# Kernel tuning notes

Measured on AMD Instinct MI355X. Metric: run time of the kernel, lower is better.

The kernel has to match this reference:

```python
import jax, jax.numpy as jnp
import numpy as np

B, N, H, D, L = 4, 1024, 8, 256, 4
SVD, NSP = 16, 512
DK = D // H
EPS = 1e-6


def setup_inputs() -> dict:
    key = jax.random.key(0)
    ks = jax.random.split(key, 40)
    p = {}
    p["x"] = jax.random.normal(ks[0], (B, N, D), jnp.float32)
    p["in_degrees"] = jax.random.randint(ks[1], (N,), 0, N)
    p["out_degrees"] = jax.random.randint(ks[2], (N,), 0, N)
    p["spatial_pos"] = jax.random.randint(ks[3], (N, N), 0, NSP)
    p["svd_emb"] = jax.random.normal(ks[4], (N, 2 * SVD), jnp.float32)
    # embedding tables (padding_idx=0 -> zero row)
    p["in_deg_emb"] = (0.02 * jax.random.normal(ks[5], (N, D), jnp.float32)).at[0].set(0.0)
    p["out_deg_emb"] = (0.02 * jax.random.normal(ks[6], (N, D), jnp.float32)).at[0].set(0.0)
    p["spatial_emb"] = (0.02 * jax.random.normal(ks[7], (NSP, H), jnp.float32)).at[0].set(0.0)
    # SVD linear (stored [in, out]; y = x @ W + b)
    p["W_svd"] = 0.02 * jax.random.normal(ks[8], (2 * SVD, D), jnp.float32)
    p["b_svd"] = jnp.zeros((D,), jnp.float32)
    # per-layer stacked transformer params
    names = ["Wq", "Wk", "Wv", "Wa", "W1", "W2"]
    for i, nm in enumerate(names):
        p[nm] = 0.05 * jax.random.normal(ks[9 + i], (L, D, D), jnp.float32)
    for nm in ["bq", "bk", "bv", "ba", "b1", "b2", "ln1_b", "ln2_b"]:
        p[nm] = jnp.zeros((L, D), jnp.float32)
    p["ln1_g"] = jnp.ones((L, D), jnp.float32)
    p["ln2_g"] = jnp.ones((L, D), jnp.float32)
    return p


def _ln(x, g, b):
    mu = jnp.mean(x, axis=-1, keepdims=True)
    var = jnp.mean(jnp.square(x - mu), axis=-1, keepdims=True)
    return (x - mu) * jax.lax.rsqrt(var + EPS) * g + b


def _forward(x, svd_emb, W_svd, b_svd, in_deg_emb, out_deg_emb, spatial_emb,
             Wq, bq, Wk, bk, Wv, bv, Wa, ba, ln1_g, ln1_b,
             W1, b1, W2, b2, ln2_g, ln2_b,
             in_degrees, out_degrees, spatial_pos):
    # node-level: degree embeddings ([N,D] broadcasts over batch)
    x = x + in_deg_emb[in_degrees] + out_deg_emb[out_degrees]
    # node-level: SVD embedding (deterministic sign = +1 -> concat(u, -v))
    pos = jnp.concatenate([svd_emb[:, :SVD], -svd_emb[:, SVD:]], axis=-1)
    x = x + pos @ W_svd + b_svd
    # attention-level spatial bias: [N,N,H] -> [H,N,N], broadcast over batch
    attn_bias = jnp.transpose(spatial_emb[spatial_pos], (2, 0, 1))
    scale = 1.0 / jnp.sqrt(jnp.asarray(DK, x.dtype))

    def body(h, params):
        wq, bq_, wk, bk_, wv, bv_, wa, ba_, g1, b1_, w1, bb1, w2, bb2, g2, b2_ = params
        q = (h @ wq + bq_).reshape(B, N, H, DK)
        k = (h @ wk + bk_).reshape(B, N, H, DK)
        v = (h @ wv + bv_).reshape(B, N, H, DK)
        # scores [B,H,N,N] + spatial bias [H,N,N]
        scores = jnp.einsum('bqhd,bkhd->bhqk', q, k) * scale + attn_bias
        attn = jax.nn.softmax(scores, axis=-1)
        o = jnp.einsum('bhqk,bkhd->bqhd', attn, v).reshape(B, N, D)
        h = _ln(h + o @ wa + ba_, g1, b1_)
        f = jnp.maximum(h @ w1 + bb1, 0.0) @ w2 + bb2
        h = _ln(h + f, g2, b2_)
        return h, None

    x, _ = jax.lax.scan(body, x, (Wq, bq, Wk, bk, Wv, bv, Wa, ba, ln1_g, ln1_b,
                                  W1, b1, W2, b2, ln2_g, ln2_b))
    return x


def reference(x, svd_emb, W_svd, b_svd, in_deg_emb, out_deg_emb, spatial_emb,
              Wq, bq, Wk, bk, Wv, bv, Wa, ba, ln1_g, ln1_b,
              W1, b1, W2, b2, ln2_g, ln2_b,
              in_degrees, out_degrees, spatial_pos):
    return _forward(x, svd_emb, W_svd, b_svd, in_deg_emb, out_deg_emb, spatial_emb,
                    Wq, bq, Wk, bk, Wv, bv, Wa, ba, ln1_g, ln1_b,
                    W1, b1, W2, b2, ln2_g, ln2_b,
                    in_degrees, out_degrees, spatial_pos)
```

## Files before the change

### kernel.cpp

```cpp
#include <hip/hip_runtime.h>
#include <hip/hip_bf16.h>
#include <math.h>

#define NN 1024
#define BB 4
#define HH 8
#define DD 256
#define LL 4
#define DKK 32
#define MM 4096
#define EPSF 1e-6f
#define LOG2EF 1.4426950408889634f
#define SCLOG2E 0.2550348625f

typedef __attribute__((ext_vector_type(8))) short short8;
typedef __attribute__((ext_vector_type(4))) float f32x4;
typedef unsigned int u32;

__device__ __forceinline__ unsigned short f2bf(float f) {
    __hip_bfloat16 h = __float2bfloat16(f);
    return *(unsigned short*)&h;
}
__device__ __forceinline__ float bf2f(unsigned short u) {
    unsigned v = ((unsigned)u) << 16;
    return __builtin_bit_cast(float, v);
}

__global__ __launch_bounds__(256) void init_kernel(
    const float* __restrict__ x, const int* __restrict__ deg_in,
    const int* __restrict__ deg_out, const float* __restrict__ svd,
    const float* __restrict__ in_emb, const float* __restrict__ out_emb,
    const float* __restrict__ Wsvd, const float* __restrict__ bsvd,
    const float* __restrict__ Wq, const float* __restrict__ Wk,
    const float* __restrict__ Wv, const float* __restrict__ Wa,
    const float* __restrict__ W1, const float* __restrict__ W2,
    const int* __restrict__ sp, const float* __restrict__ spemb,
    float* __restrict__ h, short* __restrict__ hb,
    short* __restrict__ Wt, short* __restrict__ bsw)
{
    int blk = blockIdx.x;
    int tid = threadIdx.x;
    {
        int n = blk & (NN - 1);
        int di = deg_in[n], dou = deg_out[n];
        float acc = x[(size_t)blk * DD + tid] + in_emb[(size_t)di * DD + tid]
                  + out_emb[(size_t)dou * DD + tid] + bsvd[tid];
        const float* sv = &svd[n * 32];
#pragma unroll
        for (int j = 0; j < 32; ++j) {
            float v = sv[j];
            v = (j < 16) ? v : -v;
            acc += v * Wsvd[j * DD + tid];
        }
        h[(size_t)blk * DD + tid] = acc;
        hb[(size_t)blk * DD + tid] = (short)f2bf(acc);
    }
    if (blk < 384) {
        __shared__ float t[64][65];
        int z = blk >> 4, tile = blk & 15;
        int name = z >> 2;
        const float* srcs[6] = {Wq, Wk, Wv, Wa, W1, W2};
        const float* W = srcs[name] + (size_t)(z & 3) * DD * DD;
        short* dst = Wt + (size_t)z * DD * DD;
        int r0 = (tile >> 2) * 64, c0 = (tile & 3) * 64;
#pragma unroll
        for (int i = 0; i < 16; ++i) {
            int idx = i * 256 + tid;
            int r = idx >> 6, cc = idx & 63;
            t[r][cc] = W[(size_t)(r0 + r) * DD + c0 + cc];
        }
        __syncthreads();
#pragma unroll
        for (int i = 0; i < 16; ++i) {
            int idx = i * 256 + tid;
            int n = idx >> 6, kk = idx & 63;
            dst[(size_t)(c0 + n) * DD + r0 + kk] = (short)f2bf(t[kk][n]);
        }
    } else if (blk < 1408) {
        int bb = blk - 384;
        int part = bb & 3;
        int tt = (bb >> 2) * 256 + tid;
        int ln = tt & 63, kt = (tt >> 6) & 15, q16 = tt >> 10;
        int qd = ln >> 4, cc = ln & 15;
        unsigned buf[8][2];
#pragma unroll
        for (int r = 0; r < 4; ++r) {
            int row = q16 * 16 + qd * 4 + r;
            int colj = kt * 64 + part * 16 + cc;
            int pp = sp[row * NN + colj];
            float4 e0 = *(const float4*)&spemb[pp * 8];
            float4 e1 = *(const float4*)&spemb[pp * 8 + 4];
            float ev[8] = {e0.x, e0.y, e0.z, e0.w, e1.x, e1.y, e1.z, e1.w};
#pragma unroll
            for (int hh = 0; hh < 8; ++hh) {
                unsigned short u = f2bf(ev[hh] * LOG2EF);
                if (r & 1) buf[hh][r >> 1] |= ((unsigned)u) << 16;
                else       buf[hh][r >> 1] = u;
            }
        }
#pragma unroll
        for (int hh = 0; hh < 8; ++hh) {
            uint2* dst = (uint2*)&bsw[(((size_t)hh * 64 + q16) * 16 + kt) * 1024
                                      + (size_t)ln * 16 + part * 4];
            *dst = make_uint2(buf[hh][0], buf[hh][1]);
        }
    }
}

__global__ __launch_bounds__(256) void gemm_qkv_kernel(
    const short* __restrict__ A,
    const short* __restrict__ Wtq, const short* __restrict__ Wtk,
    const short* __restrict__ Wtv,
    const float* __restrict__ bq, const float* __restrict__ bk,
    const float* __restrict__ bv,
    short* __restrict__ qo, short* __restrict__ ko, short* __restrict__ vo)
{
    int z = blockIdx.z;
    const short* Wt = (z == 0) ? Wtq : (z == 1) ? Wtk : Wtv;
    const float* bs = (z == 0) ? bq : (z == 1) ? bk : bv;
    int tid = threadIdx.x, wave = tid >> 6, lane = tid & 63;
    int quad = lane >> 4, c = lane & 15;
    int m0 = blockIdx.x * 16;
    int n0 = blockIdx.y * 64 + wave * 16;
    f32x4 acc = {0.f, 0.f, 0.f, 0.f};
    const short* Ap = &A[(size_t)(m0 + c) * DD];
#pragma unroll
    for (int ks = 0; ks < 8; ++ks) {
        short8 af = *(const short8*)&Ap[ks * 32 + quad * 8];
        short8 bf = *(const short8*)&Wt[(size_t)(n0 + c) * DD + ks * 32 + quad * 8];
        acc = __builtin_amdgcn_mfma_f32_16x16x32_bf16(af, bf, acc, 0, 0, 0);
    }
    int b = m0 >> 10;
    int tok0 = (m0 & (NN - 1)) + quad * 4;
    int col = n0 + c;
    int head = col >> 5, dk = col & 31;
    int bh = b * 8 + head;
    float bv2 = bs[col];
    if (z == 2) {
        ushort4 pk;
        pk.x = f2bf(acc[0] + bv2); pk.y = f2bf(acc[1] + bv2);
        pk.z = f2bf(acc[2] + bv2); pk.w = f2bf(acc[3] + bv2);
        *(ushort4*)&vo[((size_t)bh * DKK + dk) * NN + tok0] = pk;
    } else {
        short* out = (z == 0) ? qo : ko;
        float sc = (z == 0) ? SCLOG2E : 1.0f;
#pragma unroll
        for (int r = 0; r < 4; ++r)
            out[((size_t)bh * NN + tok0 + r) * DKK + dk] =
                (short)f2bf((acc[r] + bv2) * sc);
    }
}

__global__ __launch_bounds__(512) void attn_kernel(
    const short* __restrict__ q, const short* __restrict__ k,
    const short* __restrict__ vt, const short* __restrict__ bsw,
    short* __restrict__ obuf)
{
    int blk = blockIdx.x;
    int head = blk & 7;
    int b = (blk >> 3) & 3;
    int qg = blk >> 5;
    int tid = threadIdx.x, wave = tid >> 6, lane = tid & 63;
    int quad = lane >> 4, c = lane & 15;
    int bh = b * 8 + head;
    int qt = qg * 8 + wave;
    int q0 = qt * 16;
    int m0 = b * NN + q0;

    __shared__ short Ks[2][64][32];
    __shared__ short Vs[2][32][64];
    __shared__ short P[8][16][72];
    const f32x4 zero = {0.f, 0.f, 0.f, 0.f};

    auto stage = [&](int t, int buf) {
        if (wave < 4) {
            const short* src = &k[((size_t)bh * NN + t * 64 + wave * 16 + (lane >> 2)) * DKK
                                  + (lane & 3) * 8];
            __builtin_amdgcn_global_load_lds(
                (const __attribute__((address_space(1))) u32*)src,
                (__attribute__((address_space(3))) u32*)&Ks[buf][wave * 16][0], 16, 0, 0);
        } else {
            const short* src = &vt[((size_t)bh * DKK + (wave - 4) * 8 + (lane >> 3)) * NN
                                   + t * 64 + (lane & 7) * 8];
            __builtin_amdgcn_global_load_lds(
                (const __attribute__((address_space(1))) u32*)src,
                (__attribute__((address_space(3))) u32*)&Vs[buf][(wave - 4) * 8][0], 16, 0, 0);
        }
    };

    stage(0, 0);

    short8 qf = *(const short8*)&q[((size_t)bh * NN + q0 + c) * DKK + quad * 8];
    const short* bbase = &bsw[(((size_t)head * 64 + qt) * 16) * 1024 + (size_t)lane * 16];
    short8 bc0 = *(const short8*)bbase;
    short8 bc1 = *(const short8*)(bbase + 8);

    f32x4 Oa0 = zero, Oa1 = zero;
    float lsum[4] = {0.f, 0.f, 0.f, 0.f};

    __syncthreads();

    for (int kti = 0; kti < 16; ++kti) {
        int cur = kti & 1;
        if (kti < 15) stage(kti + 1, cur ^ 1);
        short8 kf[4];
#pragma unroll
        for (int f = 0; f < 4; ++f)
            kf[f] = *(const short8*)&Ks[cur][f * 16 + c][quad * 8];
        short8 vf0[2], vf1[2];
#pragma unroll
        for (int kc = 0; kc < 2; ++kc) {
            vf0[kc] = *(const short8*)&Vs[cur][c][kc * 32 + quad * 8];
            vf1[kc] = *(const short8*)&Vs[cur][16 + c][kc * 32 + quad * 8];
        }
        f32x4 s[4];
#pragma unroll
        for (int f = 0; f < 4; ++f)
            s[f] = __builtin_amdgcn_mfma_f32_16x16x32_bf16(qf, kf[f], zero, 0, 0, 0);
        short8 bn0 = bc0, bn1 = bc1;
        if (kti < 15) {
            const short* bp = bbase + (size_t)(kti + 1) * 1024;
            bn0 = *(const short8*)bp;
            bn1 = *(const short8*)(bp + 8);
        }
#pragma unroll
        for (int f = 0; f < 4; ++f)
#pragma unroll
            for (int r = 0; r < 4; ++r) {
                int jj = f * 4 + r;
                unsigned short uu = (unsigned short)((jj < 8) ? bc0[jj] : bc1[jj - 8]);
                float p = __builtin_amdgcn_exp2f(s[f][r] + bf2f(uu));
                s[f][r] = p;
                lsum[r] += p;
            }
        bc0 = bn0; bc1 = bn1;
#pragma unroll
        for (int f = 0; f < 4; ++f)
#pragma unroll
            for (int r = 0; r < 4; ++r)
                P[wave][quad * 4 + r][f * 16 + c] = (short)f2bf(s[f][r]);
#pragma unroll
        for (int kc = 0; kc < 2; ++kc) {
            short8 pf = *(const short8*)&P[wave][c][kc * 32 + quad * 8];
            Oa0 = __builtin_amdgcn_mfma_f32_16x16x32_bf16(pf, vf0[kc], Oa0, 0, 0, 0);
            Oa1 = __builtin_amdgcn_mfma_f32_16x16x32_bf16(pf, vf1[kc], Oa1, 0, 0, 0);
        }
        __syncthreads();
    }
#pragma unroll
    for (int r = 0; r < 4; ++r)
#pragma unroll
        for (int off = 1; off < 16; off <<= 1)
            lsum[r] += __shfl_xor(lsum[r], off);
#pragma unroll
    for (int r = 0; r < 4; ++r) {
        float invl = 1.0f / lsum[r];
        int rr = quad * 4 + r;
        obuf[(size_t)(m0 + rr) * DD + head * 32 + c]      = (short)f2bf(Oa0[r] * invl);
        obuf[(size_t)(m0 + rr) * DD + head * 32 + 16 + c] = (short)f2bf(Oa1[r] * invl);
    }
}

template <int QKV>
__global__ __launch_bounds__(512) void post_kernel(
    const short* __restrict__ obuf,
    const short* __restrict__ Wta, const short* __restrict__ Wt1,
    const short* __restrict__ Wt2,
    const float* __restrict__ ba, const float* __restrict__ b1,
    const float* __restrict__ b2,
    const float* __restrict__ g1, const float* __restrict__ lb1,
    const float* __restrict__ g2, const float* __restrict__ lb2,
    float* __restrict__ h,
    const short* __restrict__ Wtqn, const short* __restrict__ Wtkn,
    const short* __restrict__ Wtvn,
    const float* __restrict__ bqn, const float* __restrict__ bkn,
    const float* __restrict__ bvn,
    short* __restrict__ qo, short* __restrict__ ko, short* __restrict__ vo)
{
    int tid = threadIdx.x, wave = tid >> 6, lane = tid & 63;
    int quad = lane >> 4, c = lane & 15;
    int m0 = blockIdx.x * 16;
    int b = m0 >> 10;
    int q0 = m0 & (NN - 1);
    int nb = wave * 32;

    __shared__ short t_in[16][264];
    __shared__ short t1s[16][264];
    __shared__ float shs[8][16][2];
    const f32x4 zero = {0.f, 0.f, 0.f, 0.f};

    {
        int row = tid >> 5, cg = tid & 31;
        *(short8*)&t_in[row][cg * 8] = *(const short8*)&obuf[(size_t)(m0 + row) * DD + cg * 8];
    }
    __syncthreads();

    f32x4 acc[2] = {zero, zero};
#pragma unroll
    for (int ks = 0; ks < 8; ++ks) {
        short8 af = *(const short8*)&t_in[c][ks * 32 + quad * 8];
#pragma unroll
        for (int f = 0; f < 2; ++f) {
            short8 bf = *(const short8*)&Wta[(size_t)(nb + f * 16 + c) * DD + ks * 32 + quad * 8];
            acc[f] = __builtin_amdgcn_mfma_f32_16x16x32_bf16(af, bf, acc[f], 0, 0, 0);
        }
    }
    float val[2][4];
    float ps[4] = {0.f,0.f,0.f,0.f}, ps2[4] = {0.f,0.f,0.f,0.f};
#pragma unroll
    for (int f = 0; f < 2; ++f) {
        int col = nb + f * 16 + c;
        float bv = ba[col];
#pragma unroll
        for (int r = 0; r < 4; ++r) {
            float v = h[(size_t)(m0 + quad * 4 + r) * DD + col] + acc[f][r] + bv;
            val[f][r] = v;
            ps[r] += v;
            ps2[r] += v * v;
        }
    }
#pragma unroll
    for (int r = 0; r < 4; ++r)
#pragma unroll
        for (int off = 1; off < 16; off <<= 1) {
            ps[r]  += __shfl_xor(ps[r], off);
            ps2[r] += __shfl_xor(ps2[r], off);
        }
    if (c == 0)
#pragma unroll
        for (int r = 0; r < 4; ++r) {
            shs[wave][quad * 4 + r][0] = ps[r];
            shs[wave][quad * 4 + r][1] = ps2[r];
        }
    __syncthreads();
    float res[2][4];
#pragma unroll
    for (int r = 0; r < 4; ++r) {
        int rr = quad * 4 + r;
        float ts = 0.f, t2 = 0.f;
#pragma unroll
        for (int w = 0; w < 8; ++w) { ts += shs[w][rr][0]; t2 += shs[w][rr][1]; }
        float mu = ts * (1.0f / DD);
        float rv = rsqrtf(t2 * (1.0f / DD) - mu * mu + EPSF);
#pragma unroll
        for (int f = 0; f < 2; ++f) {
            int col = nb + f * 16 + c;
            float nv = (val[f][r] - mu) * rv * g1[col] + lb1[col];
            res[f][r] = nv;
            t_in[rr][col] = (short)f2bf(nv);
        }
    }
    __syncthreads();
#pragma unroll
    for (int f = 0; f < 2; ++f) {
        int n0 = nb + f * 16;
        f32x4 a1 = zero;
#pragma unroll
        for (int ks = 0; ks < 8; ++ks) {
            short8 af = *(const short8*)&t_in[c][ks * 32 + quad * 8];
            short8 bf = *(const short8*)&Wt1[(size_t)(n0 + c) * DD + ks * 32 + quad * 8];
            a1 = __builtin_amdgcn_mfma_f32_16x16x32_bf16(af, bf, a1, 0, 0, 0);
        }
        float bv = b1[n0 + c];
#pragma unroll
        for (int r = 0; r < 4; ++r)
            t1s[quad * 4 + r][n0 + c] = (short)f2bf(fmaxf(a1[r] + bv, 0.f));
    }
    __syncthreads();
    f32x4 acc2[2] = {zero, zero};
#pragma unroll
    for (int ks = 0; ks < 8; ++ks) {
        short8 af = *(const short8*)&t1s[c][ks * 32 + quad * 8];
#pragma unroll
        for (int f = 0; f < 2; ++f) {
            short8 bf = *(const short8*)&Wt2[(size_t)(nb + f * 16 + c) * DD + ks * 32 + quad * 8];
            acc2[f] = __builtin_amdgcn_mfma_f32_16x16x32_bf16(af, bf, acc2[f], 0, 0, 0);
        }
    }
    float ps_2[4] = {0.f,0.f,0.f,0.f}, ps2_2[4] = {0.f,0.f,0.f,0.f};
#pragma unroll
    for (int f = 0; f < 2; ++f) {
        int col = nb + f * 16 + c;
        float bv = b2[col];
#pragma unroll
        for (int r = 0; r < 4; ++r) {
            float v = res[f][r] + acc2[f][r] + bv;
            val[f][r] = v;
            ps_2[r] += v;
            ps2_2[r] += v * v;
        }
    }
#pragma unroll
    for (int r = 0; r < 4; ++r)
#pragma unroll
        for (int off = 1; off < 16; off <<= 1) {
            ps_2[r]  += __shfl_xor(ps_2[r], off);
            ps2_2[r] += __shfl_xor(ps2_2[r], off);
        }
    __syncthreads();
    if (c == 0)
#pragma unroll
        for (int r = 0; r < 4; ++r) {
            shs[wave][quad * 4 + r][0] = ps_2[r];
            shs[wave][quad * 4 + r][1] = ps2_2[r];
        }
    __syncthreads();
#pragma unroll
    for (int r = 0; r < 4; ++r) {
        int rr = quad * 4 + r;
        float ts = 0.f, t2 = 0.f;
#pragma unroll
        for (int w = 0; w < 8; ++w) { ts += shs[w][rr][0]; t2 += shs[w][rr][1]; }
        float mu = ts * (1.0f / DD);
        float rv = rsqrtf(t2 * (1.0f / DD) - mu * mu + EPSF);
#pragma unroll
        for (int f = 0; f < 2; ++f) {
            int col = nb + f * 16 + c;
            float nv = (val[f][r] - mu) * rv * g2[col] + lb2[col];
            h[(size_t)(m0 + rr) * DD + col] = nv;
            t_in[rr][col] = (short)f2bf(nv);
        }
    }
    if (QKV == 0) return;
    __syncthreads();
    {
        int tok0 = q0 + quad * 4;
        const short* Wz[3] = {Wtqn, Wtkn, Wtvn};
        const float* bz[3] = {bqn, bkn, bvn};
#pragma unroll
        for (int z = 0; z < 3; ++z) {
#pragma unroll
            for (int f = 0; f < 2; ++f) {
                int n0 = nb + f * 16;
                f32x4 aq = zero;
#pragma unroll
                for (int ks = 0; ks < 8; ++ks) {
                    short8 af = *(const short8*)&t_in[c][ks * 32 + quad * 8];
                    short8 bf = *(const short8*)&Wz[z][(size_t)(n0 + c) * DD + ks * 32 + quad * 8];
                    aq = __builtin_amdgcn_mfma_f32_16x16x32_bf16(af, bf, aq, 0, 0, 0);
                }
                int col = n0 + c;
                int hd = col >> 5, dk = col & 31;
                int bh2 = b * 8 + hd;
                float bv2 = bz[z][col];
                if (z == 2) {
                    ushort4 pk;
                    pk.x = f2bf(aq[0] + bv2); pk.y = f2bf(aq[1] + bv2);
                    pk.z = f2bf(aq[2] + bv2); pk.w = f2bf(aq[3] + bv2);
                    *(ushort4*)&vo[((size_t)bh2 * DKK + dk) * NN + tok0] = pk;
                } else {
                    short* out = (z == 0) ? qo : ko;
                    float sc = (z == 0) ? SCLOG2E : 1.0f;
#pragma unroll
                    for (int r = 0; r < 4; ++r)
                        out[((size_t)bh2 * NN + tok0 + r) * DKK + dk] =
                            (short)f2bf((aq[r] + bv2) * sc);
                }
            }
        }
    }
}

extern "C" void kernel_launch(void* const* d_in, const int* in_sizes, int n_in,
                              void* d_out, int out_size, void* d_ws, size_t ws_size,
                              hipStream_t stream)
{
    const float* x       = (const float*)d_in[0];
    const int*   deg_in  = (const int*)d_in[1];
    const int*   deg_out = (const int*)d_in[2];
    const int*   sp      = (const int*)d_in[3];
    const float* svd     = (const float*)d_in[4];
    const float* in_emb  = (const float*)d_in[5];
    const float* out_emb = (const float*)d_in[6];
    const float* spemb   = (const float*)d_in[7];
    const float* Wsvd    = (const float*)d_in[8];
    const float* bsvd    = (const float*)d_in[9];
    const float* Wq = (const float*)d_in[10];
    const float* Wk = (const float*)d_in[11];
    const float* Wv = (const float*)d_in[12];
    const float* Wa = (const float*)d_in[13];
    const float* W1 = (const float*)d_in[14];
    const float* W2 = (const float*)d_in[15];
    const float* bq = (const float*)d_in[16];
    const float* bk = (const float*)d_in[17];
    const float* bv = (const float*)d_in[18];
    const float* ba = (const float*)d_in[19];
    const float* b1 = (const float*)d_in[20];
    const float* b2 = (const float*)d_in[21];
    const float* ln1b = (const float*)d_in[22];
    const float* ln2b = (const float*)d_in[23];
    const float* ln1g = (const float*)d_in[24];
    const float* ln2g = (const float*)d_in[25];

    float* h = (float*)d_out;
    char*  ws = (char*)d_ws;
    short* bias = (short*)ws;
    short* qb   = (short*)(ws + ((size_t)16 << 20));
    short* kb   = (short*)(ws + ((size_t)18 << 20));
    short* vtb  = (short*)(ws + ((size_t)20 << 20));
    short* obuf = (short*)(ws + ((size_t)22 << 20));
    short* hb   = (short*)(ws + ((size_t)26 << 20));
    short* Wt   = (short*)(ws + ((size_t)28 << 20));

    init_kernel<<<MM, 256, 0, stream>>>(x, deg_in, deg_out, svd, in_emb,
        out_emb, Wsvd, bsvd, Wq, Wk, Wv, Wa, W1, W2, sp, spemb, h, hb, Wt, bias);

    const size_t WSZ = (size_t)DD * DD;
    gemm_qkv_kernel<<<dim3(MM / 16, 4, 3), 256, 0, stream>>>(
        hb, Wt + 0 * WSZ, Wt + 4 * WSZ, Wt + 8 * WSZ, bq, bk, bv, qb, kb, vtb);

    for (int l = 0; l < LL; ++l) {
        const size_t bo = (size_t)l * DD;
        const short* Wta = Wt + (3 * 4 + l) * WSZ;
        const short* Wt1 = Wt + (4 * 4 + l) * WSZ;
        const short* Wt2 = Wt + (5 * 4 + l) * WSZ;

        attn_kernel<<<256, 512, 0, stream>>>(qb, kb, vtb, bias, obuf);

        if (l < LL - 1) {
            const size_t bo_n = (size_t)(l + 1) * DD;
            post_kernel<1><<<MM / 16, 512, 0, stream>>>(
                obuf, Wta, Wt1, Wt2,
                ba + bo, b1 + bo, b2 + bo,
                ln1g + bo, ln1b + bo, ln2g + bo, ln2b + bo, h,
                Wt + (0 * 4 + l + 1) * WSZ, Wt + (1 * 4 + l + 1) * WSZ,
                Wt + (2 * 4 + l + 1) * WSZ,
                bq + bo_n, bk + bo_n, bv + bo_n, qb, kb, vtb);
        } else {
            post_kernel<0><<<MM / 16, 512, 0, stream>>>(
                obuf, Wta, Wt1, Wt2,
                ba + bo, b1 + bo, b2 + bo,
                ln1g + bo, ln1b + bo, ln2g + bo, ln2b + bo, h,
                nullptr, nullptr, nullptr, nullptr, nullptr, nullptr,
                nullptr, nullptr, nullptr);
        }
    }
}
```

Baseline: 336.9 us.

## Transpose score MFMA to write P rows vectorized and use smaller attention blocks

The score MFMA operands are swapped so each lane holds a query row's scores across keys. That lets P be written to shared memory as packed ushort4 rows instead of scalar scattered stores, and the row-sum needs only two cross-quad shuffles. The spatial-bias pre-swizzle in init is re-laid-out to match the transposed score fragment. Attention blocks shrink from 8 waves to 4, with twice as many blocks, so each wave stages both K and V; this changes occupancy and the staging balance, and the correctness of the new bias layout is the main risk.

```diff
diff --git a/kernel.cpp b/kernel.cpp
--- a/kernel.cpp
+++ b/kernel.cpp
@@ -82,11 +82,11 @@
         int tt = (bb >> 2) * 256 + tid;
         int ln = tt & 63, kt = (tt >> 6) & 15, q16 = tt >> 10;
         int qd = ln >> 4, cc = ln & 15;
+        int row = q16 * 16 + cc;
         unsigned buf[8][2];
 #pragma unroll
         for (int r = 0; r < 4; ++r) {
-            int row = q16 * 16 + qd * 4 + r;
-            int colj = kt * 64 + part * 16 + cc;
+            int colj = kt * 64 + part * 16 + qd * 4 + r;
             int pp = sp[row * NN + colj];
             float4 e0 = *(const float4*)&spemb[pp * 8];
             float4 e1 = *(const float4*)&spemb[pp * 8 + 4];
@@ -151,7 +151,7 @@
     }
 }
 
-__global__ __launch_bounds__(512) void attn_kernel(
+__global__ __launch_bounds__(256) void attn_kernel(
     const short* __restrict__ q, const short* __restrict__ k,
     const short* __restrict__ vt, const short* __restrict__ bsw,
     short* __restrict__ obuf)
@@ -163,29 +163,26 @@
     int tid = threadIdx.x, wave = tid >> 6, lane = tid & 63;
     int quad = lane >> 4, c = lane & 15;
     int bh = b * 8 + head;
-    int qt = qg * 8 + wave;
+    int qt = qg * 4 + wave;
     int q0 = qt * 16;
     int m0 = b * NN + q0;
 
     __shared__ short Ks[2][64][32];
     __shared__ short Vs[2][32][64];
-    __shared__ short P[8][16][72];
+    __shared__ short P[4][16][72];
     const f32x4 zero = {0.f, 0.f, 0.f, 0.f};
 
     auto stage = [&](int t, int buf) {
-        if (wave < 4) {
-            const short* src = &k[((size_t)bh * NN + t * 64 + wave * 16 + (lane >> 2)) * DKK
-                                  + (lane & 3) * 8];
-            __builtin_amdgcn_global_load_lds(
-                (const __attribute__((address_space(1))) u32*)src,
-                (__attribute__((address_space(3))) u32*)&Ks[buf][wave * 16][0], 16, 0, 0);
-        } else {
-            const short* src = &vt[((size_t)bh * DKK + (wave - 4) * 8 + (lane >> 3)) * NN
-                                   + t * 64 + (lane & 7) * 8];
-            __builtin_amdgcn_global_load_lds(
-                (const __attribute__((address_space(1))) u32*)src,
-                (__attribute__((address_space(3))) u32*)&Vs[buf][(wave - 4) * 8][0], 16, 0, 0);
-        }
+        const short* ksrc = &k[((size_t)bh * NN + t * 64 + wave * 16 + (lane >> 2)) * DKK
+                               + (lane & 3) * 8];
+        __builtin_amdgcn_global_load_lds(
+            (const __attribute__((address_space(1))) u32*)ksrc,
+            (__attribute__((address_space(3))) u32*)&Ks[buf][wave * 16][0], 16, 0, 0);
+        const short* vsrc = &vt[((size_t)bh * DKK + wave * 8 + (lane >> 3)) * NN
+                                + t * 64 + (lane & 7) * 8];
+        __builtin_amdgcn_global_load_lds(
+            (const __attribute__((address_space(1))) u32*)vsrc,
+            (__attribute__((address_space(3))) u32*)&Vs[buf][wave * 8][0], 16, 0, 0);
     };
 
     stage(0, 0);
@@ -196,7 +193,7 @@
     short8 bc1 = *(const short8*)(bbase + 8);
 
     f32x4 Oa0 = zero, Oa1 = zero;
-    float lsum[4] = {0.f, 0.f, 0.f, 0.f};
+    float lsum = 0.f;
 
     __syncthreads();
 
@@ -216,7 +213,7 @@
         f32x4 s[4];
 #pragma unroll
         for (int f = 0; f < 4; ++f)
-            s[f] = __builtin_amdgcn_mfma_f32_16x16x32_bf16(qf, kf[f], zero, 0, 0, 0);
+            s[f] = __builtin_amdgcn_mfma_f32_16x16x32_bf16(kf[f], qf, zero, 0, 0, 0);
         short8 bn0 = bc0, bn1 = bc1;
         if (kti < 15) {
             const short* bp = bbase + (size_t)(kti + 1) * 1024;
@@ -224,21 +221,21 @@
             bn1 = *(const short8*)(bp + 8);
         }
 #pragma unroll
-        for (int f = 0; f < 4; ++f)
+        for (int f = 0; f < 4; ++f) {
+            ushort4 pk;
 #pragma unroll
             for (int r = 0; r < 4; ++r) {
                 int jj = f * 4 + r;
                 unsigned short uu = (unsigned short)((jj < 8) ? bc0[jj] : bc1[jj - 8]);
                 float p = __builtin_amdgcn_exp2f(s[f][r] + bf2f(uu));
-                s[f][r] = p;
-                lsum[r] += p;
+                lsum += p;
+                unsigned short pb = f2bf(p);
+                if (r == 0) pk.x = pb; else if (r == 1) pk.y = pb;
+                else if (r == 2) pk.z = pb; else pk.w = pb;
             }
+            *(ushort4*)&P[wave][c][f * 16 + quad * 4] = pk;
+        }
         bc0 = bn0; bc1 = bn1;
-#pragma unroll
-        for (int f = 0; f < 4; ++f)
-#pragma unroll
-            for (int r = 0; r < 4; ++r)
-                P[wave][quad * 4 + r][f * 16 + c] = (short)f2bf(s[f][r]);
 #pragma unroll
         for (int kc = 0; kc < 2; ++kc) {
             short8 pf = *(const short8*)&P[wave][c][kc * 32 + quad * 8];
@@ -247,15 +244,12 @@
         }
         __syncthreads();
     }
-#pragma unroll
-    for (int r = 0; r < 4; ++r)
-#pragma unroll
-        for (int off = 1; off < 16; off <<= 1)
-            lsum[r] += __shfl_xor(lsum[r], off);
+    lsum += __shfl_xor(lsum, 16);
+    lsum += __shfl_xor(lsum, 32);
 #pragma unroll
     for (int r = 0; r < 4; ++r) {
-        float invl = 1.0f / lsum[r];
         int rr = quad * 4 + r;
+        float invl = 1.0f / __shfl(lsum, rr);
         obuf[(size_t)(m0 + rr) * DD + head * 32 + c]      = (short)f2bf(Oa0[r] * invl);
         obuf[(size_t)(m0 + rr) * DD + head * 32 + 16 + c] = (short)f2bf(Oa1[r] * invl);
     }
@@ -515,7 +509,7 @@
         const short* Wt1 = Wt + (4 * 4 + l) * WSZ;
         const short* Wt2 = Wt + (5 * 4 + l) * WSZ;
 
-        attn_kernel<<<256, 512, 0, stream>>>(qb, kb, vtb, bias, obuf);
+        attn_kernel<<<512, 256, 0, stream>>>(qb, kb, vtb, bias, obuf);
 
         if (l < LL - 1) {
             const size_t bo_n = (size_t)(l + 1) * DD;
```

Measured after the change: 324.7 us, median of 3. 3.6% less time.
